# Optimization experiments

Measured on AMD Instinct MI355X. Metric: run time of the kernel, lower is better.

Reference implementation:

```python
import jax, jax.numpy as jnp
import numpy as np

BINS = np.array([1, 2, 3, 4, 8, 16, 32, 64], dtype=np.int32)


def setup_inputs() -> dict:
    N, G, F, H, K = 1024, 620, 20, 150, 128
    D_in = 3 * G + F  # 1880
    key = jax.random.key(0)
    ks = jax.random.split(key, 10)
    g = jax.random.normal(ks[0], (N, G), dtype=jnp.float32)
    si = jax.random.normal(ks[1], (N,), dtype=jnp.float32)
    i1 = jnp.sort(jax.random.randint(ks[2], (N,), 0, 8192)).astype(jnp.int32)
    i2 = jnp.sort(jax.random.randint(ks[3], (N,), 0, 8192)).astype(jnp.int32)
    dist_emb = jax.random.normal(ks[4], (9, F), dtype=jnp.float32) * 0.02
    W1 = jax.random.normal(ks[5], (D_in, H), dtype=jnp.float32) * (1.0 / np.sqrt(D_in))
    b1 = jnp.zeros((H,), jnp.float32)
    W2 = jax.random.normal(ks[6], (H, H), dtype=jnp.float32) * (1.0 / np.sqrt(H))
    b2 = jnp.zeros((H,), jnp.float32)
    W3 = jax.random.normal(ks[7], (H, 1), dtype=jnp.float32) * (1.0 / np.sqrt(H))
    b3 = jnp.zeros((1,), jnp.float32)
    return {"g": g, "si": si, "i1": i1, "i2": i2, "dist_emb": dist_emb,
            "W1": W1, "b1": b1, "W2": W2, "b2": b2, "W3": W3, "b3": b3, "K": K}


def reference(g, si, i1, i2, dist_emb, W1, b1, W2, b2, W3, b3, K):
    # Dropout is inference-disabled; epsilon dummy antecedent appended as last column.
    N, G = g.shape
    # span n's antecedents are spans [max(0, n-K), n); lay out as [N, K] window
    j_idx = jnp.arange(N)[:, None] - K + jnp.arange(K)[None, :]  # [N, K]
    valid = j_idx >= 0
    j = jnp.clip(j_idx, 0, N - 1)
    g_j = g[j]                      # [N, K, G] ragged gather (masked dense)
    g_i = g[:, None, :]             # [N, 1, G]
    # distance feature: bin(i.i2 - j.i1) with idx = #bins <= d
    d = i2[:, None] - i1[j]         # [N, K]
    bin_idx = jnp.searchsorted(jnp.asarray(BINS), d, side='right')
    de = dist_emb[bin_idx]          # [N, K, F]
    pairs = jnp.concatenate(
        [jnp.broadcast_to(g_i, (N, K, G)), g_j, g_i * g_j, de], axis=-1)  # [N, K, 3G+F]
    h = jax.nn.relu(jnp.einsum('nkd,dh->nkh', pairs, W1) + b1)
    h = jax.nn.relu(jnp.einsum('nkh,hm->nkm', h, W2) + b2)
    s = (jnp.einsum('nkh,ho->nko', h, W3) + b3)[..., 0]  # [N, K]
    sij = si[:, None] + si[j] + s
    sij = jnp.where(valid, sij, 0.0)
    eps = jnp.zeros((N, 1), sij.dtype)  # epsilon dummy score
    return jnp.concatenate([sij, eps], axis=-1)  # [N, K+1]
```

## Files before the change

kernel.cpp:

```cpp
#include <hip/hip_runtime.h>
#include <hip/hip_bf16.h>
#include <stdint.h>

typedef __attribute__((ext_vector_type(8))) short short8;
typedef __attribute__((ext_vector_type(4))) float float4_t;

#define N_PTS 1024
#define G_DIM 620
#define G_PAD 640
#define F_DIM 20
#define H_DIM 150
#define H_PAD 160
#define K_WIN 128
#define OUT_C (K_WIN + 1)

__device__ __forceinline__ float bf2f(short u) {
  union { unsigned int i; float f; } x;
  x.i = ((unsigned int)(unsigned short)u) << 16;
  return x.f;
}
__device__ __forceinline__ short f2bf(float f) {
  union { float f; unsigned int i; } x; x.f = f;
  unsigned int u = x.i;
  u += 0x7FFFu + ((u >> 16) & 1u);
  return (short)(u >> 16);
}
__device__ __forceinline__ short f2bf_hw(float f) {
  __hip_bfloat16 h = __float2bfloat16(f);
  union { __hip_bfloat16 h; short s; } u; u.h = h;
  return u.s;
}
__device__ __forceinline__ void gload_lds16(const void* g, void* l) {
  __builtin_amdgcn_global_load_lds(
      (const __attribute__((address_space(1))) unsigned int*)g,
      (__attribute__((address_space(3))) unsigned int*)l, 16, 0, 0);
}

__global__ void prep_pack(const float* __restrict__ g, const float* __restrict__ W1,
                          const float* __restrict__ W2, const float* __restrict__ dist_emb,
                          short* __restrict__ g_bf, short* __restrict__ W1cT,
                          short* __restrict__ W1abT, short* __restrict__ W2T,
                          float* __restrict__ deW) {
  __shared__ float lds[32 * 165];
  const int bx = blockIdx.x, tid = threadIdx.x;
  if (bx < 256) {
    const int n0 = bx * 4;
    for (int c = tid; c < 320; c += 256) {
      int r = c / 80, cc = c - r * 80;
      int n = n0 + r, d0 = cc * 8;
      short8 o;
      if (d0 + 8 <= G_DIM) {
        const float* src = g + n * G_DIM + d0;
        #pragma unroll
        for (int e = 0; e < 8; ++e) o[e] = f2bf(src[e]);
      } else {
        #pragma unroll
        for (int e = 0; e < 8; ++e) {
          int d = d0 + e;
          o[e] = (d < G_DIM) ? f2bf(g[n * G_DIM + d]) : (short)0;
        }
      }
      *(short8*)(g_bf + n * G_PAD + d0) = o;
    }
  } else if (bx < 316) {
    const int tb = bx - 256;
    const int third = tb / 20, dt = tb - third * 20;
    const int d0 = dt * 32;
    for (int c = tid; c < 1280; c += 256) {
      int dr = c / 40, ch4 = c - dr * 40;
      int dd = d0 + dr;
      int w1r = third * G_DIM + dd;
      #pragma unroll
      for (int e = 0; e < 4; ++e) {
        int h = ch4 * 4 + e;
        lds[dr * 165 + h] = (dd < G_DIM && h < H_DIM) ? W1[w1r * H_DIM + h] : 0.f;
      }
    }
    __syncthreads();
    short* outp = (third == 2) ? W1cT : (W1abT + third * H_PAD * G_PAD);
    for (int c = tid; c < 640; c += 256) {
      int h = c >> 2, ch = c & 3;
      short8 o;
      #pragma unroll
      for (int e = 0; e < 8; ++e) o[e] = f2bf(lds[(ch * 8 + e) * 165 + h]);
      *(short8*)(outp + h * G_PAD + d0 + ch * 8) = o;
    }
  } else if (bx < 320) {
    const int base = (bx - 316) * 6400;
    for (int c = tid; c < 6400; c += 256) {
      int q = base + c;
      int m = q / H_PAD, k = q - m * H_PAD;
      W2T[q] = (m < H_DIM && k < H_DIM) ? f2bf(W2[k * H_DIM + m]) : (short)0;
    }
  } else {
    for (int c = tid; c < 9 * H_PAD; c += 256) {
      int b = c / H_PAD, h = c - b * H_PAD;
      float acc = 0.f;
      if (h < H_DIM)
        for (int f = 0; f < F_DIM; ++f)
          acc += dist_emb[b * F_DIM + f] * W1[(3 * G_DIM + f) * H_DIM + h];
      deW[c] = acc;
    }
  }
}

__global__ __launch_bounds__(256) void prep_uv_mfma(
    const short* __restrict__ g_bf, const short* __restrict__ W1abT,
    const float* __restrict__ b1, float* __restrict__ U, float* __restrict__ V) {
  __shared__ __align__(16) char sA[32 * 128];
  __shared__ __align__(16) char sB[160 * 128];
  const int m0 = blockIdx.x * 32;
  const int yb = blockIdx.y * H_PAD;
  const int tid = threadIdx.x, lane = tid & 63, wid = tid >> 6;
  const int wm = wid >> 1, wn = wid & 1;
  const int lo4 = lane & 15, hi2 = lane >> 4;
  const int l8 = lane >> 3, c8 = lane & 7;
  const int xe = (c8 ^ (l8 & 7)) * 8;

  const float4_t fz = {0.f, 0.f, 0.f, 0.f};
  float4_t acc[5];
  #pragma unroll
  for (int b = 0; b < 5; ++b) acc[b] = fz;

  for (int step = 0; step < 10; ++step) {
    const int d0 = step * 64;
    {
      int row = wid * 8 + l8;
      gload_lds16(g_bf + (m0 + row) * G_PAD + d0 + xe, sA + (wid * 8) * 128);
    }
    #pragma unroll
    for (int cc = 0; cc < 5; ++cc) {
      int row = wid * 8 + cc * 32 + l8;
      gload_lds16(W1abT + (yb + row) * G_PAD + d0 + xe, sB + (wid * 8 + cc * 32) * 128);
    }
    __syncthreads();
    #pragma unroll
    for (int ks = 0; ks < 2; ++ks) {
      const int kb = ks * 64 + 16 * hi2;
      short8 af, bq[5];
      {
        int row = wm * 16 + lo4;
        af = *((const short8*)(sA + row * 128 + (kb ^ ((row & 7) << 4))));
      }
      #pragma unroll
      for (int nt = 0; nt < 5; ++nt) {
        int row = wn * 80 + nt * 16 + lo4;
        bq[nt] = *((const short8*)(sB + row * 128 + (kb ^ ((row & 7) << 4))));
      }
      #pragma unroll
      for (int nt = 0; nt < 5; ++nt)
        acc[nt] = __builtin_amdgcn_mfma_f32_16x16x32_bf16(af, bq[nt], acc[nt], 0, 0, 0);
    }
    __syncthreads();
  }

  const bool isU = (blockIdx.y == 0);
  float* O = isU ? U : V;
  #pragma unroll
  for (int r = 0; r < 4; ++r) {
    int m = m0 + wm * 16 + hi2 * 4 + r;
    #pragma unroll
    for (int nt = 0; nt < 5; ++nt) {
      int h = wn * 80 + nt * 16 + lo4;
      float v = acc[nt][r];
      if (h < H_DIM) { if (isU) v += b1[h]; } else { v = 0.f; }
      O[m * H_PAD + h] = v;
    }
  }
}

__global__ __launch_bounds__(256, 2) void pair_main(
    const float* __restrict__ g, const short* __restrict__ g_bf,
    const short* __restrict__ W1cT, const short* __restrict__ W2T,
    const float* __restrict__ U, const float* __restrict__ V,
    const float* __restrict__ deW, const float* __restrict__ si,
    const int* __restrict__ i1, const int* __restrict__ i2,
    const float* __restrict__ W3, const float* __restrict__ b2,
    const float* __restrict__ b3, float* __restrict__ out) {
  __shared__ __align__(16) char smem[49152];
  __shared__ __align__(16) float gi_sf[G_PAD];
  __shared__ float sj_s[K_WIN];
  __shared__ unsigned char bin_su[K_WIN];
  __shared__ float s_buf[2][K_WIN];

  char* const B0 = smem;
  char* const B1 = smem + 20480;
  char* const Hb = smem;

  const int bid = blockIdx.x;
  const int i = ((bid & 7) << 7) | (bid >> 3);
  const int tid = threadIdx.x;
  const int lane = tid & 63;
  const int wid = tid >> 6;
  const int wm = wid >> 1, wn = wid & 1;
  const int lo4 = lane & 15, hi2 = lane >> 4;

  if (tid < 160) {
    float4_t v;
    if (tid < 155) v = *(const float4_t*)(g + i * G_DIM + tid * 4);
    else { v.x = v.y = v.z = v.w = 0.f; }
    *(float4_t*)(gi_sf + tid * 4) = v;
  }
  if (tid < K_WIN) {
    int jr = i - K_WIN + tid, jc = jr < 0 ? 0 : jr;
    int d = i2[i] - i1[jc];
    bin_su[tid] = (unsigned char)((d >= 1) + (d >= 2) + (d >= 3) + (d >= 4) +
                                  (d >= 8) + (d >= 16) + (d >= 32) + (d >= 64));
    sj_s[tid] = si[jc];
  }
  __syncthreads();

  const short* gA[4];
  #pragma unroll
  for (int mt = 0; mt < 4; ++mt) {
    int row = wm * 64 + mt * 16 + lo4;
    int jr = i - K_WIN + row, jc = jr < 0 ? 0 : jr;
    gA[mt] = g_bf + jc * G_PAD + hi2 * 8;
  }
  const int srow = tid >> 3;
  const int scb = tid & 7;

  auto loadW1 = [&](int s, short8 (&w)[5]) {
    const short* base = W1cT + s * 64 + scb * 8;
    #pragma unroll
    for (int cc = 0; cc < 5; ++cc)
      w[cc] = *(const short8*)(base + (srow + cc * 32) * G_PAD);
  };
  auto loadGJ = [&](int s, short8 (&gj)[4][2]) {
    #pragma unroll
    for (int mt = 0; mt < 4; ++mt)
      #pragma unroll
      for (int ks = 0; ks < 2; ++ks)
        gj[mt][ks] = *(const short8*)(gA[mt] + s * 64 + ks * 32);
  };
  auto writeBp = [&](int s, const short8 (&w)[5], char* B) {
    const float* gp = gi_sf + s * 64 + scb * 8;
    float4_t g0 = *(const float4_t*)(gp);
    float4_t g1 = *(const float4_t*)(gp + 4);
    #pragma unroll
    for (int cc = 0; cc < 5; ++cc) {
      int row = srow + cc * 32;
      short8 o;
      #pragma unroll
      for (int e = 0; e < 4; ++e) {
        o[e]     = f2bf_hw(bf2f(w[cc][e])     * g0[e]);
        o[e + 4] = f2bf_hw(bf2f(w[cc][e + 4]) * g1[e]);
      }
      *(short8*)(B + row * 128 + ((scb * 16) ^ ((row & 7) << 4))) = o;
    }
  };

  const float4_t fz = {0.f, 0.f, 0.f, 0.f};
  float4_t acc[4][5];
  #pragma unroll
  for (int a = 0; a < 4; ++a)
    #pragma unroll
    for (int b = 0; b < 5; ++b) acc[a][b] = fz;

  auto mfma_step = [&](const short8 (&gj)[4][2], const char* Bc) {
    #pragma unroll
    for (int ks = 0; ks < 2; ++ks) {
      const int kb = ks * 64 + hi2 * 16;
      short8 bq[5];
      #pragma unroll
      for (int nt = 0; nt < 5; ++nt) {
        int row = wn * 80 + nt * 16 + lo4;
        bq[nt] = *((const short8*)(Bc + row * 128 + (kb ^ ((row & 7) << 4))));
      }
      #pragma unroll
      for (int mt = 0; mt < 4; ++mt)
        #pragma unroll
        for (int nt = 0; nt < 5; ++nt)
          acc[mt][nt] = __builtin_amdgcn_mfma_f32_16x16x32_bf16(gj[mt][ks], bq[nt], acc[mt][nt], 0, 0, 0);
    }
  };

  short8 wA[5], wB[5], gjA[4][2], gjB[4][2];
  loadW1(0, wA); loadGJ(0, gjA);
  writeBp(0, wA, B0);
  for (int ss = 0; ss < 5; ++ss) {
    __syncthreads();
    loadW1(2 * ss + 1, wB); loadGJ(2 * ss + 1, gjB);
    mfma_step(gjA, B0);
    writeBp(2 * ss + 1, wB, B1);
    __syncthreads();
    if (ss < 4) {
      loadW1(2 * ss + 2, wA); loadGJ(2 * ss + 2, gjA);
      mfma_step(gjB, B1);
      writeBp(2 * ss + 2, wA, B0);
    } else {
      mfma_step(gjB, B1);
    }
  }
  __syncthreads();

  float uih[5];
  #pragma unroll
  for (int nt = 0; nt < 5; ++nt) uih[nt] = U[i * H_PAD + wn * 80 + nt * 16 + lo4];
  #pragma unroll
  for (int mt = 0; mt < 4; ++mt) {
    #pragma unroll
    for (int r = 0; r < 4; ++r) {
      int m = wm * 64 + mt * 16 + hi2 * 4 + r;
      int jr = i - K_WIN + m, jc = jr < 0 ? 0 : jr;
      const float* Vj = V + jc * H_PAD;
      const float* De = deW + bin_su[m] * H_PAD;
      #pragma unroll
      for (int nt = 0; nt < 5; ++nt) {
        int h = wn * 80 + nt * 16 + lo4;
        float val = acc[mt][nt][r] + uih[nt] + Vj[h] + De[h];
        val = (h < H_DIM) ? fmaxf(val, 0.f) : 0.f;
        int tile = h >> 6, hc = h & 63;
        int byte = tile * 16384 + m * 128 + ((hc * 2) ^ ((m & 7) << 4));
        *((short*)(Hb + byte)) = f2bf_hw(val);
      }
    }
  }
  {
    short8 z = {0, 0, 0, 0, 0, 0, 0, 0};
    for (int c = tid; c < 512; c += 256) {
      int row = c >> 2, cb = c & 3;
      int byte = 2 * 16384 + row * 128 + ((64 + cb * 16) ^ ((row & 7) << 4));
      *((short8*)(Hb + byte)) = z;
    }
  }
  __syncthreads();

  float4_t acc2[4][5];
  #pragma unroll
  for (int a = 0; a < 4; ++a)
    #pragma unroll
    for (int b = 0; b < 5; ++b) acc2[a][b] = fz;

  short8 bql[2][5];
  #pragma unroll
  for (int nt = 0; nt < 5; ++nt) {
    int row = wn * 80 + nt * 16 + lo4;
    bql[0][nt] = *(const short8*)(W2T + row * H_PAD + hi2 * 8);
  }
  #pragma unroll
  for (int ks = 0; ks < 5; ++ks) {
    const int cur = ks & 1;
    if (ks < 4) {
      #pragma unroll
      for (int nt = 0; nt < 5; ++nt) {
        int row = wn * 80 + nt * 16 + lo4;
        bql[cur ^ 1][nt] = *(const short8*)(W2T + row * H_PAD + (ks + 1) * 32 + hi2 * 8);
      }
    }
    short8 af[4];
    #pragma unroll
    for (int mt = 0; mt < 4; ++mt) {
      int row = wm * 64 + mt * 16 + lo4;
      int kb = (ks & 1) * 64 + hi2 * 16;
      af[mt] = *((const short8*)(Hb + (ks >> 1) * 16384 + row * 128 + (kb ^ ((row & 7) << 4))));
    }
    #pragma unroll
    for (int mt = 0; mt < 4; ++mt)
      #pragma unroll
      for (int nt = 0; nt < 5; ++nt)
        acc2[mt][nt] = __builtin_amdgcn_mfma_f32_16x16x32_bf16(af[mt], bql[cur][nt], acc2[mt][nt], 0, 0, 0);
  }

  float sp[4][4];
  #pragma unroll
  for (int mt = 0; mt < 4; ++mt)
    #pragma unroll
    for (int r = 0; r < 4; ++r) sp[mt][r] = 0.f;

  #pragma unroll
  for (int nt = 0; nt < 5; ++nt) {
    int h = wn * 80 + nt * 16 + lo4;
    float w3 = (h < H_DIM) ? W3[h] : 0.f;
    float bb = (h < H_DIM) ? b2[h] : 0.f;
    #pragma unroll
    for (int mt = 0; mt < 4; ++mt)
      #pragma unroll
      for (int r = 0; r < 4; ++r) {
        float hv = fmaxf(acc2[mt][nt][r] + bb, 0.f);
        sp[mt][r] += hv * w3;
      }
  }
  #pragma unroll
  for (int mt = 0; mt < 4; ++mt)
    #pragma unroll
    for (int r = 0; r < 4; ++r) {
      float v = sp[mt][r];
      v += __shfl_xor(v, 1);
      v += __shfl_xor(v, 2);
      v += __shfl_xor(v, 4);
      v += __shfl_xor(v, 8);
      sp[mt][r] = v;
    }
  if (lo4 == 0) {
    #pragma unroll
    for (int mt = 0; mt < 4; ++mt)
      #pragma unroll
      for (int r = 0; r < 4; ++r) {
        int m = wm * 64 + mt * 16 + hi2 * 4 + r;
        s_buf[wn][m] = sp[mt][r];
      }
  }
  __syncthreads();

  if (tid < K_WIN) {
    int m = tid;
    int jr = i - K_WIN + m;
    float sij = si[i] + sj_s[m] + s_buf[0][m] + s_buf[1][m] + b3[0];
    out[i * OUT_C + m] = (jr >= 0) ? sij : 0.f;
  }
  if (tid == K_WIN) out[i * OUT_C + K_WIN] = 0.f;
}

extern "C" void kernel_launch(void* const* d_in, const int* in_sizes, int n_in,
                              void* d_out, int out_size, void* d_ws, size_t ws_size,
                              hipStream_t stream) {
  const float* g  = (const float*)d_in[0];
  const float* si = (const float*)d_in[1];
  const int*   i1 = (const int*)d_in[2];
  const int*   i2 = (const int*)d_in[3];
  const float* de = (const float*)d_in[4];
  const float* W1 = (const float*)d_in[5];
  const float* b1 = (const float*)d_in[6];
  const float* W2 = (const float*)d_in[7];
  const float* b2 = (const float*)d_in[8];
  const float* W3 = (const float*)d_in[9];
  const float* b3 = (const float*)d_in[10];
  float* out = (float*)d_out;

  char* ws = (char*)d_ws;
  short* g_bf  = (short*)(ws);
  short* W1cT  = (short*)(ws + 1310720);
  short* W1abT = (short*)(ws + 1515520);
  short* W2T   = (short*)(ws + 1925120);
  float* U     = (float*)(ws + 1976320);
  float* V     = (float*)(ws + 2631680);
  float* deW   = (float*)(ws + 3287040);

  prep_pack<<<321, 256, 0, stream>>>(g, W1, W2, de, g_bf, W1cT, W1abT, W2T, deW);
  prep_uv_mfma<<<dim3(32, 2), 256, 0, stream>>>(g_bf, W1abT, b1, U, V);
  pair_main<<<N_PTS, 256, 0, stream>>>(g, g_bf, W1cT, W2T, U, V, deW,
                                       si, i1, i2, W3, b2, b3, out);
}
```

Measured before the change: 88.95 us.

## Fold g_i into A tiles and stage W1 via direct global-to-LDS loads

```diff
diff --git a/kernel.cpp b/kernel.cpp
--- a/kernel.cpp
+++ b/kernel.cpp
@@ -170,21 +170,23 @@
 }
 
 __global__ __launch_bounds__(256, 2) void pair_main(
-    const float* __restrict__ g, const short* __restrict__ g_bf,
-    const short* __restrict__ W1cT, const short* __restrict__ W2T,
-    const float* __restrict__ U, const float* __restrict__ V,
-    const float* __restrict__ deW, const float* __restrict__ si,
-    const int* __restrict__ i1, const int* __restrict__ i2,
-    const float* __restrict__ W3, const float* __restrict__ b2,
-    const float* __restrict__ b3, float* __restrict__ out) {
-  __shared__ __align__(16) char smem[49152];
-  __shared__ __align__(16) float gi_sf[G_PAD];
+    const short* __restrict__ g_bf, const short* __restrict__ W1cT,
+    const short* __restrict__ W2T, const float* __restrict__ U,
+    const float* __restrict__ V, const float* __restrict__ deW,
+    const float* __restrict__ si, const int* __restrict__ i1,
+    const int* __restrict__ i2, const float* __restrict__ W3,
+    const float* __restrict__ b2, const float* __restrict__ b3,
+    float* __restrict__ out) {
+  __shared__ __align__(16) char smem[73728];
+  __shared__ __align__(16) short gi_s[G_PAD];
   __shared__ float sj_s[K_WIN];
   __shared__ unsigned char bin_su[K_WIN];
   __shared__ float s_buf[2][K_WIN];
 
-  char* const B0 = smem;
-  char* const B1 = smem + 20480;
+  char* const P0 = smem;
+  char* const P1 = smem + 16384;
+  char* const B0 = smem + 32768;
+  char* const B1 = smem + 53248;
   char* const Hb = smem;
 
   const int bid = blockIdx.x;
@@ -194,13 +196,12 @@
   const int wid = tid >> 6;
   const int wm = wid >> 1, wn = wid & 1;
   const int lo4 = lane & 15, hi2 = lane >> 4;
-
-  if (tid < 160) {
-    float4_t v;
-    if (tid < 155) v = *(const float4_t*)(g + i * G_DIM + tid * 4);
-    else { v.x = v.y = v.z = v.w = 0.f; }
-    *(float4_t*)(gi_sf + tid * 4) = v;
-  }
+  const int l8 = lane >> 3, c8 = lane & 7;
+  const int xe = (c8 ^ (l8 & 7)) * 8;
+  const int tc8 = tid & 7;
+
+  if (tid < G_PAD / 8)
+    ((short8*)gi_s)[tid] = ((const short8*)(g_bf + i * G_PAD))[tid];
   if (tid < K_WIN) {
     int jr = i - K_WIN + tid, jc = jr < 0 ? 0 : jr;
     int d = i2[i] - i1[jc];
@@ -210,45 +211,42 @@
   }
   __syncthreads();
 
-  const short* gA[4];
-  #pragma unroll
-  for (int mt = 0; mt < 4; ++mt) {
-    int row = wm * 64 + mt * 16 + lo4;
-    int jr = i - K_WIN + row, jc = jr < 0 ? 0 : jr;
-    gA[mt] = g_bf + jc * G_PAD + hi2 * 8;
-  }
-  const int srow = tid >> 3;
-  const int scb = tid & 7;
-
-  auto loadW1 = [&](int s, short8 (&w)[5]) {
-    const short* base = W1cT + s * 64 + scb * 8;
-    #pragma unroll
-    for (int cc = 0; cc < 5; ++cc)
-      w[cc] = *(const short8*)(base + (srow + cc * 32) * G_PAD);
+  auto loadA = [&](int s, short8 (&gjv)[4], short8& gvv) {
+    const int d0 = s * 64;
+    gvv = *((const short8*)(gi_s + d0 + tc8 * 8));
+    #pragma unroll
+    for (int cc = 0; cc < 4; ++cc) {
+      int c = tid + 256 * cc, row = c >> 3;
+      int jr = i - K_WIN + row, jc = jr < 0 ? 0 : jr;
+      gjv[cc] = *((const short8*)(g_bf + jc * G_PAD + d0 + tc8 * 8));
+    }
   };
-  auto loadGJ = [&](int s, short8 (&gj)[4][2]) {
-    #pragma unroll
-    for (int mt = 0; mt < 4; ++mt)
-      #pragma unroll
-      for (int ks = 0; ks < 2; ++ks)
-        gj[mt][ks] = *(const short8*)(gA[mt] + s * 64 + ks * 32);
+  auto stageB = [&](int s, char* B) {
+    const int d0 = s * 64;
+    #pragma unroll
+    for (int cc = 0; cc < 5; ++cc) {
+      int row = wid * 8 + cc * 32 + l8;
+      gload_lds16(W1cT + row * G_PAD + d0 + xe, B + (wid * 8 + cc * 32) * 128);
+    }
   };
-  auto writeBp = [&](int s, const short8 (&w)[5], char* B) {
-    const float* gp = gi_sf + s * 64 + scb * 8;
-    float4_t g0 = *(const float4_t*)(gp);
-    float4_t g1 = *(const float4_t*)(gp + 4);
-    #pragma unroll
-    for (int cc = 0; cc < 5; ++cc) {
-      int row = srow + cc * 32;
-      short8 o;
-      #pragma unroll
-      for (int e = 0; e < 4; ++e) {
-        o[e]     = f2bf_hw(bf2f(w[cc][e])     * g0[e]);
-        o[e + 4] = f2bf_hw(bf2f(w[cc][e + 4]) * g1[e]);
-      }
-      *(short8*)(B + row * 128 + ((scb * 16) ^ ((row & 7) << 4))) = o;
+  auto writeP = [&](char* P, const short8 (&gjv)[4], const short8& gvv) {
+    #pragma unroll
+    for (int cc = 0; cc < 4; ++cc) {
+      int c = tid + 256 * cc, row = c >> 3;
+      short8 p;
+      #pragma unroll
+      for (int e = 0; e < 8; ++e) p[e] = f2bf_hw(bf2f(gjv[cc][e]) * bf2f(gvv[e]));
+      int byte = row * 128 + ((tc8 * 16) ^ ((row & 7) << 4));
+      *((short8*)(P + byte)) = p;
     }
   };
+
+  {
+    short8 gjv[4], gvv;
+    loadA(0, gjv, gvv);
+    stageB(0, B0);
+    writeP(P0, gjv, gvv);
+  }
 
   const float4_t fz = {0.f, 0.f, 0.f, 0.f};
   float4_t acc[4][5];
@@ -257,11 +255,27 @@
     #pragma unroll
     for (int b = 0; b < 5; ++b) acc[a][b] = fz;
 
-  auto mfma_step = [&](const short8 (&gj)[4][2], const char* Bc) {
+  for (int s = 0; s < 10; ++s) {
+    char* Pc = (s & 1) ? P1 : P0;
+    char* Bc = (s & 1) ? B1 : B0;
+    char* Pn = (s & 1) ? P0 : P1;
+    char* Bn = (s & 1) ? B0 : B1;
+    __syncthreads();
+    short8 gjv[4], gvv;
+    if (s < 9) {
+      loadA(s + 1, gjv, gvv);
+      stageB(s + 1, Bn);
+    }
+    __builtin_amdgcn_s_setprio(1);
     #pragma unroll
     for (int ks = 0; ks < 2; ++ks) {
-      const int kb = ks * 64 + hi2 * 16;
-      short8 bq[5];
+      const int kb = ks * 64 + 16 * hi2;
+      short8 af[4], bq[5];
+      #pragma unroll
+      for (int mt = 0; mt < 4; ++mt) {
+        int row = wm * 64 + mt * 16 + lo4;
+        af[mt] = *((const short8*)(Pc + row * 128 + (kb ^ ((row & 7) << 4))));
+      }
       #pragma unroll
       for (int nt = 0; nt < 5; ++nt) {
         int row = wn * 80 + nt * 16 + lo4;
@@ -271,26 +285,10 @@
       for (int mt = 0; mt < 4; ++mt)
         #pragma unroll
         for (int nt = 0; nt < 5; ++nt)
-          acc[mt][nt] = __builtin_amdgcn_mfma_f32_16x16x32_bf16(gj[mt][ks], bq[nt], acc[mt][nt], 0, 0, 0);
-    }
-  };
-
-  short8 wA[5], wB[5], gjA[4][2], gjB[4][2];
-  loadW1(0, wA); loadGJ(0, gjA);
-  writeBp(0, wA, B0);
-  for (int ss = 0; ss < 5; ++ss) {
-    __syncthreads();
-    loadW1(2 * ss + 1, wB); loadGJ(2 * ss + 1, gjB);
-    mfma_step(gjA, B0);
-    writeBp(2 * ss + 1, wB, B1);
-    __syncthreads();
-    if (ss < 4) {
-      loadW1(2 * ss + 2, wA); loadGJ(2 * ss + 2, gjA);
-      mfma_step(gjB, B1);
-      writeBp(2 * ss + 2, wA, B0);
-    } else {
-      mfma_step(gjB, B1);
-    }
+          acc[mt][nt] = __builtin_amdgcn_mfma_f32_16x16x32_bf16(af[mt], bq[nt], acc[mt][nt], 0, 0, 0);
+    }
+    __builtin_amdgcn_s_setprio(0);
+    if (s < 9) writeP(Pn, gjv, gvv);
   }
   __syncthreads();
 
@@ -355,11 +353,13 @@
       int kb = (ks & 1) * 64 + hi2 * 16;
       af[mt] = *((const short8*)(Hb + (ks >> 1) * 16384 + row * 128 + (kb ^ ((row & 7) << 4))));
     }
+    __builtin_amdgcn_s_setprio(1);
     #pragma unroll
     for (int mt = 0; mt < 4; ++mt)
       #pragma unroll
       for (int nt = 0; nt < 5; ++nt)
         acc2[mt][nt] = __builtin_amdgcn_mfma_f32_16x16x32_bf16(af[mt], bql[cur][nt], acc2[mt][nt], 0, 0, 0);
+    __builtin_amdgcn_s_setprio(0);
   }
 
   float sp[4][4];
@@ -439,6 +439,6 @@
 
   prep_pack<<<321, 256, 0, stream>>>(g, W1, W2, de, g_bf, W1cT, W1abT, W2T, deW);
   prep_uv_mfma<<<dim3(32, 2), 256, 0, stream>>>(g_bf, W1abT, b1, U, V);
-  pair_main<<<N_PTS, 256, 0, stream>>>(g, g_bf, W1cT, W2T, U, V, deW,
+  pair_main<<<N_PTS, 256, 0, stream>>>(g_bf, W1cT, W2T, U, V, deW,
                                        si, i1, i2, W3, b2, b3, out);
 }
```

Result: faster. 71.83 us (-19.2%).
